# Kernel optimization log

Measured on AMD Instinct MI355X. Metric: run time of the kernel, lower is better.

Reference implementation:

```python
import jax, jax.numpy as jnp
from jax import lax
import numpy as np

B, H, W, C = 8, 128, 128, 256
NUM_ANCHORS_PER_LOC = 15  # len(scales)=5 * len(ratios)=3


def _conv(x, w, b, padding):
    # NHWC conv, HWIO kernel (matches keras Conv2D)
    y = lax.conv_general_dilated(x, w, window_strides=(1, 1), padding=padding,
                                 dimension_numbers=('NHWC', 'HWIO', 'NHWC'))
    return y + b


def setup_inputs() -> dict:
    key = jax.random.key(0)
    ks = jax.random.split(key, 5)
    std = jnp.float32(0.01)  # TruncatedNormal(0, 0.01) init in original
    x = jax.random.normal(ks[0], (B, H, W, C), jnp.float32)
    w_shared = jax.random.normal(ks[1], (3, 3, C, 512), jnp.float32) * std
    b_shared = jnp.zeros((512,), jnp.float32)
    w_cls = jax.random.normal(ks[2], (1, 1, 512, 2 * NUM_ANCHORS_PER_LOC), jnp.float32) * std
    b_cls = jnp.zeros((2 * NUM_ANCHORS_PER_LOC,), jnp.float32)
    w_reg = jax.random.normal(ks[3], (1, 1, 512, 4 * NUM_ANCHORS_PER_LOC), jnp.float32) * std
    b_reg = jnp.zeros((4 * NUM_ANCHORS_PER_LOC,), jnp.float32)
    return {'x': x, 'w_shared': w_shared, 'b_shared': b_shared,
            'w_cls': w_cls, 'b_cls': b_cls, 'w_reg': w_reg, 'b_reg': b_reg}


def reference(x, w_shared, b_shared, w_cls, b_cls, w_reg, b_reg):
    # shared 3x3 conv + relu6
    shared = jnp.clip(_conv(x, w_shared, b_shared, 'SAME'), 0.0, 6.0)
    # class branch: 1x1 conv -> [B, num_anchors, 2] -> softmax
    cls = _conv(shared, w_cls, b_cls, 'VALID')
    rpn_class_logits = cls.reshape(cls.shape[0], -1, 2)
    rpn_probs = jax.nn.softmax(rpn_class_logits, axis=-1)
    reg = _conv(shared, w_reg, b_reg, 'VALID')
    rpn_deltas = reg.reshape(reg.shape[0], -1, 4)
    return (rpn_class_logits, rpn_probs, rpn_deltas)
```

## Files before the change

### kernel.cpp

```cpp
#include <hip/hip_runtime.h>
#include <stdint.h>


#define HH 128
#define WW 128
#define CIN 256

typedef __attribute__((ext_vector_type(8))) short short8;
typedef __attribute__((ext_vector_type(4))) float f32x4;

#define LDS_B_OFF 66560
#define LDS_TOTAL 132096

static __device__ __forceinline__ unsigned short f2bf(float f) {
    uint32_t u = __float_as_uint(f);
    uint32_t r = (u + 0x7FFFu + ((u >> 16) & 1u)) >> 16;
    return (unsigned short)r;
}

__global__ __launch_bounds__(256) void prep_wk(const float* __restrict__ w,
                                               unsigned short* __restrict__ wk) {
    __shared__ unsigned short t[32][130];
    const int c = blockIdx.x >> 2, nh = blockIdx.x & 3;
    const int dydx = c >> 3, kc = c & 7;
    #pragma unroll
    for (int e = 0; e < 16; ++e) {
        int idx = e * 256 + threadIdx.x;
        int kk = idx >> 7, n0 = idx & 127;
        float v = w[((size_t)(dydx * 256 + kc * 32 + kk)) * 512 + nh * 128 + n0];
        t[kk][n0] = f2bf(v);
    }
    __syncthreads();
    #pragma unroll
    for (int e = 0; e < 16; ++e) {
        int idx = e * 256 + threadIdx.x;
        int n0 = idx >> 5, kk = idx & 31;
        int n = nh * 128 + n0;
        int kks = kk ^ (((n >> 1) & 3) << 3);
        wk[(size_t)c * 16384 + (size_t)n * 32 + kks] = t[kk][n0];
    }
}

__global__ __launch_bounds__(256) void prep_wbr(const float* __restrict__ wc,
                                                const float* __restrict__ wr,
                                                unsigned short* __restrict__ wbr) {
    int t = blockIdx.x * 256 + threadIdx.x;
    int n = t >> 9, k = t & 511;
    float v = 0.f;
    if (n < 30) v = wc[k * 30 + n];
    else if (n >= 32 && n < 92) v = wr[k * 60 + (n - 32)];
    wbr[n * 512 + k] = f2bf(v);
}

__global__ __launch_bounds__(512, 2) void rpn_fused(
    const float* __restrict__ x, const unsigned short* __restrict__ wk,
    const float* __restrict__ bsh, const unsigned short* __restrict__ wbr,
    const float* __restrict__ bcls, const float* __restrict__ breg,
    float* __restrict__ out)
{
    extern __shared__ char smem[];
    const int tid = threadIdx.x;
    const int lane = tid & 63;
    const int wid = tid >> 6;
    const int wm = wid >> 2, wn = wid & 3;
    const int l15 = lane & 15, l4 = lane >> 4;
    const int blk = blockIdx.x;
    const int bb = blk >> 7, h = blk & 127;

    const int n0 = wn * 128 + l15;
    const int bofs = n0 * 64 + ((l4 * 16) ^ (((n0 >> 1) & 3) << 4));

    f32x4 acc[4][8];
    #pragma unroll
    for (int i = 0; i < 4; ++i)
        #pragma unroll
        for (int j = 0; j < 8; ++j) acc[i][j] = (f32x4){0.f, 0.f, 0.f, 0.f};

    {
        const char* src = reinterpret_cast<const char*>(wk) + tid * 16;
        char* dst = smem + LDS_B_OFF + tid * 16;
        #pragma unroll
        for (int r = 0; r < 4; ++r)
            __builtin_amdgcn_global_load_lds(
                reinterpret_cast<const uint32_t*>(src + r * 8192),
                reinterpret_cast<uint32_t*>(dst + r * 8192), 16, 0, 0);
    }

    int g = 0;
    for (int dy = 0; dy < 3; ++dy) {
        {
            const int hp = h + dy - 1;
            const bool hin = (hp >= 0) && (hp < HH);
            const float* xrow = x + ((size_t)(bb * HH + hp)) * WW * CIN;
            for (int u = tid; u < 130 * 32; u += 512) {
                const int pos = u >> 5, c8 = u & 31;
                const int wc = pos - 1;
                float4 f0 = make_float4(0.f,0.f,0.f,0.f), f1 = make_float4(0.f,0.f,0.f,0.f);
                if (hin && (unsigned)wc < WW) {
                    const float4* p = reinterpret_cast<const float4*>(xrow + (size_t)wc * CIN + c8 * 8);
                    f0 = p[0]; f1 = p[1];
                }
                short8 v;
                v[0]=(short)f2bf(f0.x); v[1]=(short)f2bf(f0.y);
                v[2]=(short)f2bf(f0.z); v[3]=(short)f2bf(f0.w);
                v[4]=(short)f2bf(f1.x); v[5]=(short)f2bf(f1.y);
                v[6]=(short)f2bf(f1.z); v[7]=(short)f2bf(f1.w);
                *reinterpret_cast<short8*>(smem + pos * 512 + ((c8 * 16) ^ ((pos & 7) << 4))) = v;
            }
        }
        for (int i = 0; i < 24; ++i, ++g) {
            const int nxt = g + 1;
            if (nxt < 72) {
                const char* src = reinterpret_cast<const char*>(wk) + (size_t)nxt * 32768 + tid * 16;
                char* dst = smem + LDS_B_OFF + ((nxt & 1) << 15) + tid * 16;
                #pragma unroll
                for (int r = 0; r < 4; ++r)
                    __builtin_amdgcn_global_load_lds(
                        reinterpret_cast<const uint32_t*>(src + r * 8192),
                        reinterpret_cast<uint32_t*>(dst + r * 8192), 16, 0, 0);
                if (i == 0) asm volatile("s_waitcnt vmcnt(4) lgkmcnt(0)" ::: "memory");
                else        asm volatile("s_waitcnt vmcnt(4)" ::: "memory");
            } else {
                asm volatile("s_waitcnt vmcnt(0) lgkmcnt(0)" ::: "memory");
            }
            __builtin_amdgcn_s_barrier();
            asm volatile("" ::: "memory");

            const int dx = (g >> 3) % 3;
            const int kc = g & 7;
            const char* bbuf = smem + LDS_B_OFF + ((g & 1) << 15);

            const int r0 = wm * 64 + l15 + dx;
            const int asw = ((kc * 32 + l4 * 8) * 2) ^ ((r0 & 7) << 4);
            short8 af0 = *reinterpret_cast<const short8*>(smem + (r0     ) * 512 + asw);
            short8 af1 = *reinterpret_cast<const short8*>(smem + (r0 + 16) * 512 + asw);
            short8 af2 = *reinterpret_cast<const short8*>(smem + (r0 + 32) * 512 + asw);
            short8 af3 = *reinterpret_cast<const short8*>(smem + (r0 + 48) * 512 + asw);

            __builtin_amdgcn_s_setprio(1);
            #pragma unroll
            for (int nf = 0; nf < 8; ++nf) {
                short8 bfv = *reinterpret_cast<const short8*>(bbuf + bofs + nf * 1024);
                acc[0][nf] = __builtin_amdgcn_mfma_f32_16x16x32_bf16(af0, bfv, acc[0][nf], 0, 0, 0);
                acc[1][nf] = __builtin_amdgcn_mfma_f32_16x16x32_bf16(af1, bfv, acc[1][nf], 0, 0, 0);
                acc[2][nf] = __builtin_amdgcn_mfma_f32_16x16x32_bf16(af2, bfv, acc[2][nf], 0, 0, 0);
                acc[3][nf] = __builtin_amdgcn_mfma_f32_16x16x32_bf16(af3, bfv, acc[3][nf], 0, 0, 0);
            }
            __builtin_amdgcn_s_setprio(0);
            __builtin_amdgcn_s_barrier();
            asm volatile("" ::: "memory");
        }
    }

    __syncthreads();
    #pragma unroll
    for (int nf = 0; nf < 8; ++nf) {
        const int ch = wn * 128 + nf * 16 + l15;
        const float bv = bsh[ch];
        #pragma unroll
        for (int mf = 0; mf < 4; ++mf) {
            #pragma unroll
            for (int r = 0; r < 4; ++r) {
                const int pos = wm * 64 + mf * 16 + l4 * 4 + r;
                float v = acc[mf][nf][r] + bv;
                v = fminf(fmaxf(v, 0.f), 6.f);
                *reinterpret_cast<unsigned short*>(
                    smem + pos * 1024 + ((ch * 2) ^ ((pos & 7) << 4))) = f2bf(v);
            }
        }
    }
    __syncthreads();

    f32x4 bacc[6];
    #pragma unroll
    for (int nf = 0; nf < 6; ++nf) bacc[nf] = (f32x4){0.f,0.f,0.f,0.f};
    const int pos0 = wid * 16;
    #pragma unroll 4
    for (int kstep = 0; kstep < 16; ++kstep) {
        const int ch = kstep * 32 + l4 * 8;
        const int posr = pos0 + l15;
        short8 af = *reinterpret_cast<const short8*>(
            smem + posr * 1024 + ((ch * 2) ^ ((posr & 7) << 4)));
        #pragma unroll
        for (int nf = 0; nf < 6; ++nf) {
            const int n = nf * 16 + l15;
            short8 bfr = *reinterpret_cast<const short8*>(wbr + n * 512 + ch);
            bacc[nf] = __builtin_amdgcn_mfma_f32_16x16x32_bf16(af, bfr, bacc[nf], 0, 0, 0);
        }
    }

    const size_t rowbase = (size_t)h * 128;
    #pragma unroll
    for (int nf = 0; nf < 2; ++nf) {
        const int n = nf * 16 + l15;
        const float bias = (n < 30) ? bcls[n] : 0.f;
        #pragma unroll
        for (int r = 0; r < 4; ++r) {
            float v = bacc[nf][r] + bias;
            float vo = __shfl_xor(v, 1);
            float mx = fmaxf(v, vo);
            float e  = __expf(v - mx), eo = __expf(vo - mx);
            float p  = e / (e + eo);
            if (n < 30) {
                const int wc = pos0 + l4 * 4 + r;
                const size_t anchor = (rowbase + wc) * 15 + (n >> 1);
                const size_t idx = (size_t)bb * 491520 + anchor * 2 + (n & 1);
                out[idx] = v;
                out[3932160 + idx] = p;
            }
        }
    }
    #pragma unroll
    for (int nf = 2; nf < 6; ++nf) {
        const int n = nf * 16 + l15;
        const int nr = n - 32;
        const float bias = (nr < 60) ? breg[nr] : 0.f;
        #pragma unroll
        for (int r = 0; r < 4; ++r) {
            float v = bacc[nf][r] + bias;
            if (nr < 60) {
                const int wc = pos0 + l4 * 4 + r;
                const size_t anchor = (rowbase + wc) * 15 + (nr >> 2);
                out[7864320 + (size_t)bb * 983040 + anchor * 4 + (nr & 3)] = v;
            }
        }
    }
}

extern "C" void kernel_launch(void* const* d_in, const int* in_sizes, int n_in,
                              void* d_out, int out_size, void* d_ws, size_t ws_size,
                              hipStream_t stream) {
    const float* x    = (const float*)d_in[0];
    const float* wsh  = (const float*)d_in[1];
    const float* bsh  = (const float*)d_in[2];
    const float* wcls = (const float*)d_in[3];
    const float* bcls = (const float*)d_in[4];
    const float* wreg = (const float*)d_in[5];
    const float* breg = (const float*)d_in[6];
    float* out = (float*)d_out;

    unsigned short* wk  = (unsigned short*)d_ws;
    unsigned short* wbr = wk + 1179648;

    prep_wk <<<288, 256, 0, stream>>>(wsh, wk);
    prep_wbr<<<192, 256, 0, stream>>>(wcls, wreg, wbr);

    hipFuncSetAttribute((const void*)rpn_fused,
                        hipFuncAttributeMaxDynamicSharedMemorySize, LDS_TOTAL);
    rpn_fused<<<1024, 512, LDS_TOTAL, stream>>>(x, wk, bsh, wbr, bcls, breg, out);
}
```

Measured before the change: 602.5 us.

## Split weight tiles into half-stages with 4-slot ring and deeper prefetch

Weight-tile loads into LDS are split into half-size pieces (half of the N columns per stage) in a 4-slot ring with three halves in flight, replacing the double-buffered full-tile scheme. The prep kernel permutes the N ordering so each half-slot holds contiguous per-wave column groups. B fragments are loaded into registers before the wait and barrier, so LDS reads overlap outstanding global loads and MFMA runs in two 16-instruction bursts per K step. This is meant to hide global-to-LDS latency behind compute, at the cost of twice as many barriers per K step and hand-tuned waitcnt counts that must match the issue order exactly.

```diff
diff --git a/kernel.cpp b/kernel.cpp
--- a/kernel.cpp
+++ b/kernel.cpp
@@ -35,9 +35,10 @@
     for (int e = 0; e < 16; ++e) {
         int idx = e * 256 + threadIdx.x;
         int n0 = idx >> 5, kk = idx & 31;
-        int n = nh * 128 + n0;
-        int kks = kk ^ (((n >> 1) & 3) << 3);
-        wk[(size_t)c * 16384 + (size_t)n * 32 + kks] = t[kk][n0];
+        int nf = n0 >> 4, l = n0 & 15;
+        int np = ((nf >> 2) << 8) | (nh << 6) | ((nf & 3) << 4) | l;
+        int kks = kk ^ (((np >> 1) & 3) << 3);
+        wk[(size_t)c * 16384 + (size_t)np * 32 + kks] = t[kk][n0];
     }
 }
 
@@ -67,8 +68,7 @@
     const int blk = blockIdx.x;
     const int bb = blk >> 7, h = blk & 127;
 
-    const int n0 = wn * 128 + l15;
-    const int bofs = n0 * 64 + ((l4 * 16) ^ (((n0 >> 1) & 3) << 4));
+    const int bofs = (wn * 64 + l15) * 64 + ((l4 * 16) ^ (((l15 >> 1) & 3) << 4));
 
     f32x4 acc[4][8];
     #pragma unroll
@@ -76,17 +76,24 @@
         #pragma unroll
         for (int j = 0; j < 8; ++j) acc[i][j] = (f32x4){0.f, 0.f, 0.f, 0.f};
 
-    {
-        const char* src = reinterpret_cast<const char*>(wk) + tid * 16;
-        char* dst = smem + LDS_B_OFF + tid * 16;
-        #pragma unroll
-        for (int r = 0; r < 4; ++r)
-            __builtin_amdgcn_global_load_lds(
-                reinterpret_cast<const uint32_t*>(src + r * 8192),
-                reinterpret_cast<uint32_t*>(dst + r * 8192), 16, 0, 0);
-    }
-
-    int g = 0;
+#define ISSUE_HALF(hh)                                                            \
+    if ((hh) < 144) {                                                             \
+        const char* s_ = reinterpret_cast<const char*>(wk) + ((size_t)(hh) << 14) \
+                         + tid * 16;                                              \
+        char* d_ = smem + LDS_B_OFF + (((hh) & 3) << 14) + tid * 16;              \
+        __builtin_amdgcn_global_load_lds(reinterpret_cast<const uint32_t*>(s_),   \
+                                         reinterpret_cast<uint32_t*>(d_), 16, 0, 0); \
+        __builtin_amdgcn_global_load_lds(reinterpret_cast<const uint32_t*>(s_ + 8192), \
+                                         reinterpret_cast<uint32_t*>(d_ + 8192), 16, 0, 0); \
+    }
+
+#define WAITV(tt)                                                          \
+    if ((tt) <= 140)      asm volatile("s_waitcnt vmcnt(4)" ::: "memory"); \
+    else if ((tt) == 141) asm volatile("s_waitcnt vmcnt(2)" ::: "memory"); \
+    else                  asm volatile("s_waitcnt vmcnt(0)" ::: "memory");
+
+    ISSUE_HALF(0); ISSUE_HALF(1); ISSUE_HALF(2);
+
     for (int dy = 0; dy < 3; ++dy) {
         {
             const int hp = h + dy - 1;
@@ -108,47 +115,81 @@
                 *reinterpret_cast<short8*>(smem + pos * 512 + ((c8 * 16) ^ ((pos & 7) << 4))) = v;
             }
         }
-        for (int i = 0; i < 24; ++i, ++g) {
-            const int nxt = g + 1;
-            if (nxt < 72) {
-                const char* src = reinterpret_cast<const char*>(wk) + (size_t)nxt * 32768 + tid * 16;
-                char* dst = smem + LDS_B_OFF + ((nxt & 1) << 15) + tid * 16;
-                #pragma unroll
-                for (int r = 0; r < 4; ++r)
-                    __builtin_amdgcn_global_load_lds(
-                        reinterpret_cast<const uint32_t*>(src + r * 8192),
-                        reinterpret_cast<uint32_t*>(dst + r * 8192), 16, 0, 0);
-                if (i == 0) asm volatile("s_waitcnt vmcnt(4) lgkmcnt(0)" ::: "memory");
-                else        asm volatile("s_waitcnt vmcnt(4)" ::: "memory");
-            } else {
-                asm volatile("s_waitcnt vmcnt(0) lgkmcnt(0)" ::: "memory");
-            }
-            __builtin_amdgcn_s_barrier();
-            asm volatile("" ::: "memory");
-
-            const int dx = (g >> 3) % 3;
-            const int kc = g & 7;
-            const char* bbuf = smem + LDS_B_OFF + ((g & 1) << 15);
-
+        if (dy == 0) asm volatile("s_waitcnt vmcnt(4) lgkmcnt(0)" ::: "memory");
+        else         asm volatile("s_waitcnt lgkmcnt(0)" ::: "memory");
+        __builtin_amdgcn_sched_barrier(0);
+        __builtin_amdgcn_s_barrier();
+
+        for (int i = 0; i < 24; ++i) {
+            const int g = dy * 24 + i;
+            const int t0 = 2 * g;
+            const int dx = i >> 3, kc = i & 7;
+
+            const char* slot0 = smem + LDS_B_OFF + ((t0 & 3) << 14);
             const int r0 = wm * 64 + l15 + dx;
-            const int asw = ((kc * 32 + l4 * 8) * 2) ^ ((r0 & 7) << 4);
+            const int asw = ((kc * 32 + l4 * 8) << 1) ^ ((r0 & 7) << 4);
             short8 af0 = *reinterpret_cast<const short8*>(smem + (r0     ) * 512 + asw);
             short8 af1 = *reinterpret_cast<const short8*>(smem + (r0 + 16) * 512 + asw);
             short8 af2 = *reinterpret_cast<const short8*>(smem + (r0 + 32) * 512 + asw);
             short8 af3 = *reinterpret_cast<const short8*>(smem + (r0 + 48) * 512 + asw);
-
+            short8 b0 = *reinterpret_cast<const short8*>(slot0 + bofs);
+            short8 b1 = *reinterpret_cast<const short8*>(slot0 + bofs + 1024);
+            short8 b2 = *reinterpret_cast<const short8*>(slot0 + bofs + 2048);
+            short8 b3 = *reinterpret_cast<const short8*>(slot0 + bofs + 3072);
+            ISSUE_HALF(t0 + 3);
+            WAITV(t0);
+            __builtin_amdgcn_s_barrier();
+            asm volatile("s_waitcnt lgkmcnt(0)" ::: "memory");
+            __builtin_amdgcn_sched_barrier(0);
             __builtin_amdgcn_s_setprio(1);
-            #pragma unroll
-            for (int nf = 0; nf < 8; ++nf) {
-                short8 bfv = *reinterpret_cast<const short8*>(bbuf + bofs + nf * 1024);
-                acc[0][nf] = __builtin_amdgcn_mfma_f32_16x16x32_bf16(af0, bfv, acc[0][nf], 0, 0, 0);
-                acc[1][nf] = __builtin_amdgcn_mfma_f32_16x16x32_bf16(af1, bfv, acc[1][nf], 0, 0, 0);
-                acc[2][nf] = __builtin_amdgcn_mfma_f32_16x16x32_bf16(af2, bfv, acc[2][nf], 0, 0, 0);
-                acc[3][nf] = __builtin_amdgcn_mfma_f32_16x16x32_bf16(af3, bfv, acc[3][nf], 0, 0, 0);
-            }
+            acc[0][0] = __builtin_amdgcn_mfma_f32_16x16x32_bf16(af0, b0, acc[0][0], 0, 0, 0);
+            acc[1][0] = __builtin_amdgcn_mfma_f32_16x16x32_bf16(af1, b0, acc[1][0], 0, 0, 0);
+            acc[2][0] = __builtin_amdgcn_mfma_f32_16x16x32_bf16(af2, b0, acc[2][0], 0, 0, 0);
+            acc[3][0] = __builtin_amdgcn_mfma_f32_16x16x32_bf16(af3, b0, acc[3][0], 0, 0, 0);
+            acc[0][1] = __builtin_amdgcn_mfma_f32_16x16x32_bf16(af0, b1, acc[0][1], 0, 0, 0);
+            acc[1][1] = __builtin_amdgcn_mfma_f32_16x16x32_bf16(af1, b1, acc[1][1], 0, 0, 0);
+            acc[2][1] = __builtin_amdgcn_mfma_f32_16x16x32_bf16(af2, b1, acc[2][1], 0, 0, 0);
+            acc[3][1] = __builtin_amdgcn_mfma_f32_16x16x32_bf16(af3, b1, acc[3][1], 0, 0, 0);
+            acc[0][2] = __builtin_amdgcn_mfma_f32_16x16x32_bf16(af0, b2, acc[0][2], 0, 0, 0);
+            acc[1][2] = __builtin_amdgcn_mfma_f32_16x16x32_bf16(af1, b2, acc[1][2], 0, 0, 0);
+            acc[2][2] = __builtin_amdgcn_mfma_f32_16x16x32_bf16(af2, b2, acc[2][2], 0, 0, 0);
+            acc[3][2] = __builtin_amdgcn_mfma_f32_16x16x32_bf16(af3, b2, acc[3][2], 0, 0, 0);
+            acc[0][3] = __builtin_amdgcn_mfma_f32_16x16x32_bf16(af0, b3, acc[0][3], 0, 0, 0);
+            acc[1][3] = __builtin_amdgcn_mfma_f32_16x16x32_bf16(af1, b3, acc[1][3], 0, 0, 0);
+            acc[2][3] = __builtin_amdgcn_mfma_f32_16x16x32_bf16(af2, b3, acc[2][3], 0, 0, 0);
+            acc[3][3] = __builtin_amdgcn_mfma_f32_16x16x32_bf16(af3, b3, acc[3][3], 0, 0, 0);
             __builtin_amdgcn_s_setprio(0);
             __builtin_amdgcn_s_barrier();
-            asm volatile("" ::: "memory");
+
+            const char* slot1 = smem + LDS_B_OFF + (((t0 + 1) & 3) << 14);
+            short8 b4 = *reinterpret_cast<const short8*>(slot1 + bofs);
+            short8 b5 = *reinterpret_cast<const short8*>(slot1 + bofs + 1024);
+            short8 b6 = *reinterpret_cast<const short8*>(slot1 + bofs + 2048);
+            short8 b7 = *reinterpret_cast<const short8*>(slot1 + bofs + 3072);
+            ISSUE_HALF(t0 + 4);
+            WAITV(t0 + 1);
+            __builtin_amdgcn_s_barrier();
+            asm volatile("s_waitcnt lgkmcnt(0)" ::: "memory");
+            __builtin_amdgcn_sched_barrier(0);
+            __builtin_amdgcn_s_setprio(1);
+            acc[0][4] = __builtin_amdgcn_mfma_f32_16x16x32_bf16(af0, b4, acc[0][4], 0, 0, 0);
+            acc[1][4] = __builtin_amdgcn_mfma_f32_16x16x32_bf16(af1, b4, acc[1][4], 0, 0, 0);
+            acc[2][4] = __builtin_amdgcn_mfma_f32_16x16x32_bf16(af2, b4, acc[2][4], 0, 0, 0);
+            acc[3][4] = __builtin_amdgcn_mfma_f32_16x16x32_bf16(af3, b4, acc[3][4], 0, 0, 0);
+            acc[0][5] = __builtin_amdgcn_mfma_f32_16x16x32_bf16(af0, b5, acc[0][5], 0, 0, 0);
+            acc[1][5] = __builtin_amdgcn_mfma_f32_16x16x32_bf16(af1, b5, acc[1][5], 0, 0, 0);
+            acc[2][5] = __builtin_amdgcn_mfma_f32_16x16x32_bf16(af2, b5, acc[2][5], 0, 0, 0);
+            acc[3][5] = __builtin_amdgcn_mfma_f32_16x16x32_bf16(af3, b5, acc[3][5], 0, 0, 0);
+            acc[0][6] = __builtin_amdgcn_mfma_f32_16x16x32_bf16(af0, b6, acc[0][6], 0, 0, 0);
+            acc[1][6] = __builtin_amdgcn_mfma_f32_16x16x32_bf16(af1, b6, acc[1][6], 0, 0, 0);
+            acc[2][6] = __builtin_amdgcn_mfma_f32_16x16x32_bf16(af2, b6, acc[2][6], 0, 0, 0);
+            acc[3][6] = __builtin_amdgcn_mfma_f32_16x16x32_bf16(af3, b6, acc[3][6], 0, 0, 0);
+            acc[0][7] = __builtin_amdgcn_mfma_f32_16x16x32_bf16(af0, b7, acc[0][7], 0, 0, 0);
+            acc[1][7] = __builtin_amdgcn_mfma_f32_16x16x32_bf16(af1, b7, acc[1][7], 0, 0, 0);
+            acc[2][7] = __builtin_amdgcn_mfma_f32_16x16x32_bf16(af2, b7, acc[2][7], 0, 0, 0);
+            acc[3][7] = __builtin_amdgcn_mfma_f32_16x16x32_bf16(af3, b7, acc[3][7], 0, 0, 0);
+            __builtin_amdgcn_s_setprio(0);
+            __builtin_amdgcn_s_barrier();
         }
     }
 
```

Result: no change. 611.8 us (+1.5%).
